# Optimization experiments

Measured on AMD Instinct MI355X. Metric: run time of the kernel, lower is better.

The kernel has to match this reference:

```python
import jax, jax.numpy as jnp
import numpy as np

B, P, V = 32, 32, 200          # batch, minPockets, vertices per pocket
NF, NT, NR, NROT = 4, 16, 5, 16
TR = NT * NR                   # 80 kernel bins
MAX_RHO = 12.0
NLIG = 7
TWO_PI = 2.0 * np.pi


def _initial_polar_grid():
    grid_rho = np.linspace(0.0, MAX_RHO, NR + 1)[1:]
    grid_theta = np.linspace(0.0, TWO_PI, NT + 1)[:-1]
    gr, gt = np.meshgrid(grid_rho, grid_theta)
    return gr.T.flatten().astype(np.float32), gt.T.flatten().astype(np.float32)


def _glorot(k, shape):
    lim = np.sqrt(6.0 / (shape[-2] + shape[-1]))
    return jax.random.uniform(k, shape, jnp.float32, -lim, lim)


def setup_inputs() -> dict:
    key = jax.random.key(0)
    ks = jax.random.split(key, 8)
    input_feat = jax.random.normal(ks[0], (B, P, V, NF), jnp.float32)
    rho_coords = jax.random.uniform(ks[1], (B, P, V, 1), jnp.float32) * MAX_RHO
    theta_coords = jax.random.uniform(ks[2], (B, P, V, 1), jnp.float32) * TWO_PI
    mask = jnp.ones((B, P, V, 1), jnp.float32)
    gr, gt = _initial_polar_grid()
    mu_rho = jnp.tile(jnp.asarray(gr)[None], (NF, 1))        # [F,TR]
    mu_theta = jnp.tile(jnp.asarray(gt)[None], (NF, 1))      # [F,TR]
    sigma_rho = jnp.full((NF, TR), MAX_RHO / 8.0, jnp.float32)
    sigma_theta = jnp.ones((NF, TR), jnp.float32)
    W_conv = _glorot(ks[3], (NF, TR, TR))
    b_conv = jnp.zeros((NF, TR), jnp.float32)
    W1 = _glorot(ks[4], (NF * TR, TR)); b1 = jnp.zeros((TR,), jnp.float32)
    W2 = _glorot(ks[5], (TR * TR, 64)); b2 = jnp.zeros((64,), jnp.float32)
    W3 = _glorot(ks[6], (64, NLIG));    b3 = jnp.zeros((NLIG,), jnp.float32)
    bn = lambda d: (jnp.ones((d,), jnp.float32), jnp.zeros((d,), jnp.float32),
                    jnp.zeros((d,), jnp.float32), jnp.ones((d,), jnp.float32))
    bn1_g, bn1_b, bn1_m, bn1_v = bn(NF * TR)
    bn2_g, bn2_b, bn2_m, bn2_v = bn(TR)
    bn3_g, bn3_b, bn3_m, bn3_v = bn(64)
    return dict(input_feat=input_feat, rho_coords=rho_coords, theta_coords=theta_coords,
                mask=mask, mu_rho=mu_rho, sigma_rho=sigma_rho, mu_theta=mu_theta,
                sigma_theta=sigma_theta, W_conv=W_conv, b_conv=b_conv, W1=W1, b1=b1,
                bn1_g=bn1_g, bn1_b=bn1_b, bn1_m=bn1_m, bn1_v=bn1_v,
                bn2_g=bn2_g, bn2_b=bn2_b, bn2_m=bn2_m, bn2_v=bn2_v,
                W2=W2, b2=b2, bn3_g=bn3_g, bn3_b=bn3_b, bn3_m=bn3_m, bn3_v=bn3_v,
                W3=W3, b3=b3)


def _bn(x, g, b, m, v, eps=1e-3):
    return (x - m) * (g * jax.lax.rsqrt(v + eps)) + b


def _conv_layer(input_feat, rho, theta, mask, mu_rho, sigma_rho, mu_theta, sigma_theta,
                W_conv, b_conv, eps=1e-5):
    # rho/theta/mask: [B,P,V,1]; mu/sigma: [F,TR]; feat: [B,P,V,F]
    # rho Gaussian is rotation-invariant -> compute once.  [B,P,V,F,TR]
    rho_g = jnp.exp(-jnp.square(rho[..., None] - mu_rho) / (jnp.square(sigma_rho) + eps))
    offs = (TWO_PI / NROT) * jnp.arange(NROT, dtype=jnp.float32)

    def step(best, off):
        th = jnp.mod(theta + off, TWO_PI)
        th_g = jnp.exp(-jnp.square(th[..., None] - mu_theta) / (jnp.square(sigma_theta) + eps))
        g = rho_g * th_g * mask[..., None]                      # [B,P,V,F,TR]
        g = g / (jnp.sum(g, axis=2, keepdims=True) + eps)       # normalize over vertices
        desc = jnp.einsum('bpvft,bpvf->bpft', g, input_feat)    # [B,P,F,TR]
        conv = jnp.einsum('bpft,ftu->bpfu', desc, W_conv) + b_conv
        return jnp.maximum(best, conv), None

    init = jnp.full((B, P, NF, TR), -jnp.inf, jnp.float32)
    best, _ = jax.lax.scan(step, init, offs)
    return best                                                  # [B,P,F,TR]


def reference(input_feat, rho_coords, theta_coords, mask, mu_rho, sigma_rho, mu_theta,
              sigma_theta, W_conv, b_conv, W1, b1, bn1_g, bn1_b, bn1_m, bn1_v,
              bn2_g, bn2_b, bn2_m, bn2_v, W2, b2, bn3_g, bn3_b, bn3_m, bn3_v, W3, b3):
    conv = _conv_layer(input_feat, rho_coords, theta_coords, mask, mu_rho, sigma_rho,
                       mu_theta, sigma_theta, W_conv, b_conv)
    x = conv.reshape(B, P, NF * TR)
    x = jax.nn.relu(_bn(x, bn1_g, bn1_b, bn1_m, bn1_v))
    x = x @ W1 + b1                                              # [B,P,TR]
    x = jax.nn.relu(_bn(x, bn2_g, bn2_b, bn2_m, bn2_v))
    cov = jnp.einsum('bpi,bpj->bij', x, x) / jnp.float32(P)      # CovarLayer [B,TR,TR]
    x = cov.reshape(B, TR * TR)
    x = jax.nn.relu(x @ W2 + b2)                                 # Dense(64, relu)
    x = _bn(x, bn3_g, bn3_b, bn3_m, bn3_v)
    return x @ W3 + b3                                           # [B, NLIG]
```

## Files before the change

kernel.cpp:

```cpp
#include <hip/hip_runtime.h>
#include <math.h>

#define B_    32
#define P_    32
#define V_    200
#define NF_   4
#define TR_   80
#define NROT_ 16
#define NLIG_ 7
#define NTH_  1024
#define PKT_  512

#define WSLOTS 33
#define CSTR   828
#define CTOT   (16 * CSTR)
#define RSTR   84
#define AUXN   5376

static constexpr float TWO_PI_F  = 6.2831854820251465f;
static constexpr float DELTA_F   = 0.39269909262657166f;

__global__ __launch_bounds__(NTH_, 4) void masif_conv_kernel(
    const float* __restrict__ feat, const float* __restrict__ rho,
    const float* __restrict__ theta, const float* __restrict__ mask,
    const float* __restrict__ mu_rho, const float* __restrict__ sigma_rho,
    const float* __restrict__ mu_theta, const float* __restrict__ sigma_theta,
    const float* __restrict__ W_conv, const float* __restrict__ b_conv,
    const float* __restrict__ W1, const float* __restrict__ b1,
    const float* __restrict__ bn1_g, const float* __restrict__ bn1_b,
    const float* __restrict__ bn1_m, const float* __restrict__ bn1_v,
    const float* __restrict__ bn2_g, const float* __restrict__ bn2_b,
    const float* __restrict__ bn2_m, const float* __restrict__ bn2_v,
    float* __restrict__ x2out)
{
    __shared__ __align__(16) float s_C[2][CTOT];
    __shared__ __align__(16) float s_aux[2][AUXN];
    __shared__ float s_mu[5], s_isr[5];
    __shared__ float s_ist1;
    __shared__ int   s_cnt[2][16], s_start[2][17];
    __shared__ int   s_whist[2][4][16];

    const int tid = threadIdx.x;
    const int pk  = tid >> 9;
    const int lt  = tid & 511;
    const int bp  = blockIdx.x * 2 + pk;
    const size_t vb = (size_t)bp * V_;

    float* Cp = s_C[pk];
    float* Ax = s_aux[pk];

    float*  stg_th  = Ax;
    float*  stg_rho = Ax + 200;
    float*  stg_msk = Ax + 400;
    float4* stg_f4  = (float4*)(Ax + 608);
    float*  Vp      = Ax + 1408;

    for (int i = lt; i < V_; i += PKT_) {
        stg_th[i]  = theta[vb + i];
        stg_rho[i] = rho[vb + i];
        stg_msk[i] = mask[vb + i];
        stg_f4[i]  = ((const float4*)(feat + vb * NF_))[i];
    }
    if (tid < 5) {
        s_mu[tid] = mu_rho[tid * 16];
        float sg = sigma_rho[tid * 16];
        s_isr[tid] = 1.0f / (sg * sg + 1e-5f);
    }
    if (tid == 5) { float sg = sigma_theta[0]; s_ist1 = 1.0f / (sg * sg + 1e-5f); }
    if (tid >= 64 && tid < 96) ((int*)s_cnt)[tid - 64] = 0;
    __syncthreads();

    int myb = 0;
    if (lt < V_) {
        float th = stg_th[lt];
        int r0 = (int)ceilf((TWO_PI_F - th) / DELTA_F);
        int lo = r0 - 2; if (lo < 1) lo = 1;
        int rs = 16;
        #pragma unroll
        for (int d = 0; d < 5; ++d) {
            int r = lo + d;
            if (r < 16 && th + (float)r * DELTA_F >= TWO_PI_F) { rs = r; break; }
        }
        myb = rs - 1;
        atomicAdd(&s_cnt[pk][myb], 1);
    }

    int rkw = 0;
    if (lt < 256) {
        const unsigned long long below = (1ULL << (tid & 63)) - 1ULL;
        const int wv = lt >> 6;
        for (int b = 0; b < 16; ++b) {
            bool p = (lt < V_) && (myb == b);
            unsigned long long m = __ballot(p);
            if (p) rkw = __popcll(m & below);
            if ((tid & 63) == b) s_whist[pk][wv][b] = __popcll(m);
        }
    }
    __syncthreads();
    if (lt == 0) {
        int run = 0;
        for (int k = 0; k < 16; ++k) { s_start[pk][k] = run; run += s_cnt[pk][k]; }
        s_start[pk][16] = run;
    }
    __syncthreads();

    {
        float4 z4 = make_float4(0.f, 0.f, 0.f, 0.f);
        float4* C4 = (float4*)Cp;
        for (int e = lt; e < CTOT / 4; e += PKT_) C4[e] = z4;
    }
    if (lt < V_) {
        int rk = rkw;
        for (int w = 0; w < (lt >> 6); ++w) rk += s_whist[pk][w][myb];
        int pos = s_start[pk][myb] + rk;
        float th = stg_th[lt];
        float mk = stg_msk[lt];
        float4 f4 = stg_f4[lt];
        float rv = stg_rho[lt];
        float R[5];
        #pragma unroll
        for (int i = 0; i < 5; ++i) {
            float d = rv - s_mu[i];
            R[i] = __expf(-d * d * s_isr[i]);
        }
        *(float4*)&Vp[pos * 12 + 0] = make_float4(R[0], R[1], R[2], R[3]);
        *(float4*)&Vp[pos * 12 + 4] = make_float4(R[4], th, f4.x * mk, f4.y * mk);
        *(float4*)&Vp[pos * 12 + 8] = make_float4(f4.z * mk, f4.w * mk, mk, 0.0f);
    }
    __syncthreads();

    {
        const int team = lt >> 5, t32 = lt & 31;
        const int w = team - 1 + t32;
        if (t32 < 20 && w >= 0 && w < WSLOTS) {
            const float ist = s_ist1;
            const float nf = (float)(team - 25 + t32);
            const int v0 = s_start[pk][team], v1 = s_start[pk][team + 1];
            float acc[25];
            #pragma unroll
            for (int i = 0; i < 25; ++i) acc[i] = 0.0f;
            for (int v = v0; v < v1; ++v) {
                float4 ra = *(const float4*)&Vp[v * 12 + 0];
                float4 rb = *(const float4*)&Vp[v * 12 + 4];
                float4 rc = *(const float4*)&Vp[v * 12 + 8];
                float q  = fmaf(nf, DELTA_F, rb.y);
                float wg = __expf(-q * q * ist);
                float R[5]  = {ra.x, ra.y, ra.z, ra.w, rb.x};
                float ch[5] = {rb.z, rb.w, rc.x, rc.y, rc.z};
                #pragma unroll
                for (int c = 0; c < 5; ++c) {
                    float t = wg * ch[c];
                    #pragma unroll
                    for (int i = 0; i < 5; ++i)
                        acc[c * 5 + i] = fmaf(t, R[i], acc[c * 5 + i]);
                }
            }
            float* dst = Cp + team * CSTR + w * 25;
            #pragma unroll
            for (int i = 0; i < 25; ++i) dst[i] = acc[i];
        }
    }
    __syncthreads();

    {
        float2* C2 = (float2*)Cp;
        for (int e = lt; e < CSTR / 2; e += PKT_) {
            float2 g[16];
            #pragma unroll
            for (int tk = 0; tk < 16; ++tk) g[tk] = C2[tk * (CSTR / 2) + e];
            #pragma unroll
            for (int tk = 1; tk < 16; ++tk) {
                g[tk].x += g[tk - 1].x; g[tk].y += g[tk - 1].y;
            }
            #pragma unroll
            for (int tk = 1; tk < 16; ++tk) C2[tk * (CSTR / 2) + e] = g[tk];
        }
    }
    __syncthreads();

    {
        const float* Tb = Cp + 15 * CSTR;
        int r   = (lt >= 320) ? 1 : 0;
        int bin = lt - r * 320;
        #pragma unroll
        for (int it = 0; it < 10; ++it) {
            const int j1  = bin & 15;
            const int ci1 = bin >> 4;
            const int c1  = (ci1 * 13) >> 6;
            const int i1  = ci1 - c1 * 5;
            const int sD = ci1, sS = 20 + i1;
            const int wT = r - j1 + 24;
            const bool pT = (wT <= 32);
            const int wTc = pT ? wT : 32;
            const float* Tp = Tb + wTc * 25;
            float tD = Tp[sD], tS = Tp[sS];
            float D = pT ? tD : 0.0f;
            float S = pT ? tS : 0.0f;
            if (r > 0) {
                const float* Cr = Cp + (r - 1) * CSTR;
                const float* Up = Cr + wTc * 25;
                float uD = Up[sD], uS = Up[sS];
                if (pT) { D -= uD; S -= uS; }
                const int wW = wT - 16;
                const bool pW = (wW >= 0);
                const int wWc = pW ? wW : 0;
                const float* Wp = Cr + wWc * 25;
                float wD = Wp[sD], wS = Wp[sS];
                if (pW) { D += wD; S += wS; }
            }
            Ax[r * (4 * RSTR) + c1 * RSTR + i1 * 16 + j1] = D / (S + 1e-5f);
            bin += 192; r += 1;
            if (bin >= 320) { bin -= 320; r += 1; }
        }
    }
    __syncthreads();

    float* s_pool2 = Cp;
    float* s_x1    = Cp + 1280;
    float* s_part  = Cp + 1600;

    if (lt < 320) {
        const int g  = lt / 80;
        const int s  = lt - g * 80;
        const int cf = s / 20;
        const int uq = s - cf * 20;
        const int u0 = uq * 4;
        const float* Wf = W_conv + (size_t)cf * TR_ * TR_ + u0;
        const float* r0 = Ax + (4 * g) * (4 * RSTR) + cf * RSTR;
        float4 a0 = make_float4(0.f, 0.f, 0.f, 0.f);
        float4 a1 = a0, a2 = a0, a3 = a0;
        #pragma unroll 4
        for (int kq = 0; kq < 20; ++kq) {
            const int k = kq * 4;
            float4 d0 = *(const float4*)&r0[k];
            float4 d1 = *(const float4*)&r0[(4 * RSTR) + k];
            float4 d2 = *(const float4*)&r0[(8 * RSTR) + k];
            float4 d3 = *(const float4*)&r0[(12 * RSTR) + k];
            float4 w0 = *(const float4*)&Wf[(size_t)(k + 0) * TR_];
            float4 w1 = *(const float4*)&Wf[(size_t)(k + 1) * TR_];
            float4 w2 = *(const float4*)&Wf[(size_t)(k + 2) * TR_];
            float4 w3 = *(const float4*)&Wf[(size_t)(k + 3) * TR_];
            a0.x = fmaf(d0.x,w0.x, fmaf(d0.y,w1.x, fmaf(d0.z,w2.x, fmaf(d0.w,w3.x, a0.x))));
            a0.y = fmaf(d0.x,w0.y, fmaf(d0.y,w1.y, fmaf(d0.z,w2.y, fmaf(d0.w,w3.y, a0.y))));
            a0.z = fmaf(d0.x,w0.z, fmaf(d0.y,w1.z, fmaf(d0.z,w2.z, fmaf(d0.w,w3.z, a0.z))));
            a0.w = fmaf(d0.x,w0.w, fmaf(d0.y,w1.w, fmaf(d0.z,w2.w, fmaf(d0.w,w3.w, a0.w))));
            a1.x = fmaf(d1.x,w0.x, fmaf(d1.y,w1.x, fmaf(d1.z,w2.x, fmaf(d1.w,w3.x, a1.x))));
            a1.y = fmaf(d1.x,w0.y, fmaf(d1.y,w1.y, fmaf(d1.z,w2.y, fmaf(d1.w,w3.y, a1.y))));
            a1.z = fmaf(d1.x,w0.z, fmaf(d1.y,w1.z, fmaf(d1.z,w2.z, fmaf(d1.w,w3.z, a1.z))));
            a1.w = fmaf(d1.x,w0.w, fmaf(d1.y,w1.w, fmaf(d1.z,w2.w, fmaf(d1.w,w3.w, a1.w))));
            a2.x = fmaf(d2.x,w0.x, fmaf(d2.y,w1.x, fmaf(d2.z,w2.x, fmaf(d2.w,w3.x, a2.x))));
            a2.y = fmaf(d2.x,w0.y, fmaf(d2.y,w1.y, fmaf(d2.z,w2.y, fmaf(d2.w,w3.y, a2.y))));
            a2.z = fmaf(d2.x,w0.z, fmaf(d2.y,w1.z, fmaf(d2.z,w2.z, fmaf(d2.w,w3.z, a2.z))));
            a2.w = fmaf(d2.x,w0.w, fmaf(d2.y,w1.w, fmaf(d2.z,w2.w, fmaf(d2.w,w3.w, a2.w))));
            a3.x = fmaf(d3.x,w0.x, fmaf(d3.y,w1.x, fmaf(d3.z,w2.x, fmaf(d3.w,w3.x, a3.x))));
            a3.y = fmaf(d3.x,w0.y, fmaf(d3.y,w1.y, fmaf(d3.z,w2.y, fmaf(d3.w,w3.y, a3.y))));
            a3.z = fmaf(d3.x,w0.z, fmaf(d3.y,w1.z, fmaf(d3.z,w2.z, fmaf(d3.w,w3.z, a3.z))));
            a3.w = fmaf(d3.x,w0.w, fmaf(d3.y,w1.w, fmaf(d3.z,w2.w, fmaf(d3.w,w3.w, a3.w))));
        }
        float4 m;
        m.x = fmaxf(fmaxf(a0.x, a1.x), fmaxf(a2.x, a3.x));
        m.y = fmaxf(fmaxf(a0.y, a1.y), fmaxf(a2.y, a3.y));
        m.z = fmaxf(fmaxf(a0.z, a1.z), fmaxf(a2.z, a3.z));
        m.w = fmaxf(fmaxf(a0.w, a1.w), fmaxf(a2.w, a3.w));
        *(float4*)&s_pool2[g * 320 + cf * TR_ + u0] = m;
    }
    __syncthreads();

    if (lt < 320) {
        float best = fmaxf(fmaxf(s_pool2[lt], s_pool2[320 + lt]),
                           fmaxf(s_pool2[640 + lt], s_pool2[960 + lt]));
        best += b_conv[lt];
        float x1 = (best - bn1_m[lt]) * (bn1_g[lt] * rsqrtf(bn1_v[lt] + 1e-3f))
                   + bn1_b[lt];
        s_x1[lt] = fmaxf(x1, 0.0f);
    }
    __syncthreads();
    for (int q = lt; q < 640; q += PKT_) {
        const int c = q / TR_;
        const int ue = q - c * TR_;
        float p = 0.0f;
        const int i0 = c * 40;
        #pragma unroll 8
        for (int i = i0; i < i0 + 40; ++i)
            p = fmaf(s_x1[i], W1[(size_t)i * TR_ + ue], p);
        s_part[q] = p;
    }
    __syncthreads();
    if (lt < TR_) {
        float h = b1[lt];
        #pragma unroll
        for (int c = 0; c < 8; ++c) h += s_part[c * TR_ + lt];
        float x2 = (h - bn2_m[lt]) * (bn2_g[lt] * rsqrtf(bn2_v[lt] + 1e-3f))
                   + bn2_b[lt];
        x2out[(size_t)bp * TR_ + lt] = fmaxf(x2, 0.0f);
    }
}

__global__ __launch_bounds__(256) void masif_head_partial(
    const float* __restrict__ x2,
    const float* __restrict__ W2,
    float* __restrict__ hpart)
{
    __shared__ __align__(16) float s_x[P_ * TR_];
    __shared__ __align__(16) float s_cov[10 * TR_];
    __shared__ float s_red[4][64];

    const int tid = threadIdx.x;
    const int b = blockIdx.x >> 3, c = blockIdx.x & 7;

    for (int i = tid; i < P_ * TR_; i += 256)
        s_x[i] = x2[(size_t)b * P_ * TR_ + i];
    __syncthreads();

    for (int o = tid; o < 800; o += 256) {
        int il = o / TR_, j = o - il * TR_;
        int i = c * 10 + il;
        float s = 0.0f;
        #pragma unroll 4
        for (int p = 0; p < P_; ++p)
            s = fmaf(s_x[p * TR_ + i], s_x[p * TR_ + j], s);
        s_cov[o] = s * (1.0f / (float)P_);
    }
    __syncthreads();

    {
        const int o = tid & 63, sub = tid >> 6;
        float acc = 0.0f;
        const int q0 = sub * 200;
        const size_t gbase = (size_t)(c * 800) * 64 + o;
        #pragma unroll 8
        for (int q = q0; q < q0 + 200; ++q)
            acc = fmaf(s_cov[q], W2[gbase + (size_t)q * 64], acc);
        s_red[sub][o] = acc;
    }
    __syncthreads();
    if (tid < 64)
        hpart[(size_t)b * 512 + c * 64 + tid] =
            s_red[0][tid] + s_red[1][tid] + s_red[2][tid] + s_red[3][tid];
}

__global__ __launch_bounds__(64) void masif_head_final(
    const float* __restrict__ hpart,
    const float* __restrict__ b2,
    const float* __restrict__ bn3_g, const float* __restrict__ bn3_b,
    const float* __restrict__ bn3_m, const float* __restrict__ bn3_v,
    const float* __restrict__ W3, const float* __restrict__ b3,
    float* __restrict__ out)
{
    __shared__ float s_h[64];
    const int tid = threadIdx.x;
    const int b = blockIdx.x;

    float h = b2[tid];
    #pragma unroll
    for (int c = 0; c < 8; ++c) h += hpart[(size_t)b * 512 + c * 64 + tid];
    h = fmaxf(h, 0.0f);
    s_h[tid] = (h - bn3_m[tid]) * (bn3_g[tid] * rsqrtf(bn3_v[tid] + 1e-3f))
               + bn3_b[tid];
    __syncthreads();

    if (tid < NLIG_) {
        float y = b3[tid];
        #pragma unroll
        for (int k = 0; k < 64; ++k)
            y = fmaf(s_h[k], W3[k * NLIG_ + tid], y);
        out[b * NLIG_ + tid] = y;
    }
}

extern "C" void kernel_launch(void* const* d_in, const int* in_sizes, int n_in,
                              void* d_out, int out_size, void* d_ws, size_t ws_size,
                              hipStream_t stream)
{
    const float* feat      = (const float*)d_in[0];
    const float* rho       = (const float*)d_in[1];
    const float* theta     = (const float*)d_in[2];
    const float* mask      = (const float*)d_in[3];
    const float* mu_rho    = (const float*)d_in[4];
    const float* sigma_rho = (const float*)d_in[5];
    const float* mu_theta  = (const float*)d_in[6];
    const float* sigma_th  = (const float*)d_in[7];
    const float* W_conv    = (const float*)d_in[8];
    const float* b_conv    = (const float*)d_in[9];
    const float* W1        = (const float*)d_in[10];
    const float* b1        = (const float*)d_in[11];
    const float* bn1_g     = (const float*)d_in[12];
    const float* bn1_b     = (const float*)d_in[13];
    const float* bn1_m     = (const float*)d_in[14];
    const float* bn1_v     = (const float*)d_in[15];
    const float* bn2_g     = (const float*)d_in[16];
    const float* bn2_b     = (const float*)d_in[17];
    const float* bn2_m     = (const float*)d_in[18];
    const float* bn2_v     = (const float*)d_in[19];
    const float* W2        = (const float*)d_in[20];
    const float* b2        = (const float*)d_in[21];
    const float* bn3_g     = (const float*)d_in[22];
    const float* bn3_b     = (const float*)d_in[23];
    const float* bn3_m     = (const float*)d_in[24];
    const float* bn3_v     = (const float*)d_in[25];
    const float* W3        = (const float*)d_in[26];
    const float* b3        = (const float*)d_in[27];

    float* x2ws  = (float*)d_ws;
    float* hpart = (float*)d_ws + (size_t)B_ * P_ * TR_;

    masif_conv_kernel<<<dim3(B_ * P_ / 2), dim3(NTH_), 0, stream>>>(
        feat, rho, theta, mask, mu_rho, sigma_rho, mu_theta, sigma_th,
        W_conv, b_conv, W1, b1,
        bn1_g, bn1_b, bn1_m, bn1_v, bn2_g, bn2_b, bn2_m, bn2_v, x2ws);

    masif_head_partial<<<dim3(B_ * 8), dim3(256), 0, stream>>>(x2ws, W2, hpart);

    masif_head_final<<<dim3(B_), dim3(64), 0, stream>>>(
        hpart, b2, bn3_g, bn3_b, bn3_m, bn3_v, W3, b3, (float*)d_out);
}
```

Baseline: 64.08 us.

## Rebalance conv accumulation and W_conv GEMM work across all block threads

The explicit zeroing pass over the accumulation buffer is removed. Out-of-band window slots are now zero-filled by the accumulation loop itself, which is rewritten as a strided loop over team/window items instead of a fixed lane mapping. The W_conv matvec-plus-max stage now spreads 2560 smaller items (2 outputs × 2 rotations each) over all 1024 threads covering both pockets, rather than 320 threads per pocket each doing 16 accumulators. This raises thread utilisation and lowers per-thread register pressure, at the cost of more index arithmetic, a wider 8-way max reduction, and repeated W_conv loads.

After: 94.06 us. 46.8% more time.

```diff
diff --git a/kernel.cpp b/kernel.cpp
--- a/kernel.cpp
+++ b/kernel.cpp
@@ -104,11 +104,6 @@
     }
     __syncthreads();
 
-    {
-        float4 z4 = make_float4(0.f, 0.f, 0.f, 0.f);
-        float4* C4 = (float4*)Cp;
-        for (int e = lt; e < CTOT / 4; e += PKT_) C4[e] = z4;
-    }
     if (lt < V_) {
         int rk = rkw;
         for (int w = 0; w < (lt >> 6); ++w) rk += s_whist[pk][w][myb];
@@ -129,12 +124,14 @@
     }
     __syncthreads();
 
-    {
-        const int team = lt >> 5, t32 = lt & 31;
-        const int w = team - 1 + t32;
-        if (t32 < 20 && w >= 0 && w < WSLOTS) {
+    for (int item = lt; item < 16 * WSLOTS; item += PKT_) {
+        const int team = item / WSLOTS;
+        const int w    = item - team * WSLOTS;
+        const int l    = w - team + 1;
+        float* dst = Cp + team * CSTR + w * 25;
+        if (l >= 0 && l < 20) {
             const float ist = s_ist1;
-            const float nf = (float)(team - 25 + t32);
+            const float nf = (float)(w - 24);
             const int v0 = s_start[pk][team], v1 = s_start[pk][team + 1];
             float acc[25];
             #pragma unroll
@@ -155,9 +152,11 @@
                         acc[c * 5 + i] = fmaf(t, R[i], acc[c * 5 + i]);
                 }
             }
-            float* dst = Cp + team * CSTR + w * 25;
             #pragma unroll
             for (int i = 0; i < 25; ++i) dst[i] = acc[i];
+        } else {
+            #pragma unroll
+            for (int i = 0; i < 25; ++i) dst[i] = 0.0f;
         }
     }
     __syncthreads();
@@ -215,64 +214,53 @@
     }
     __syncthreads();
 
-    float* s_pool2 = Cp;
-    float* s_x1    = Cp + 1280;
-    float* s_part  = Cp + 1600;
-
-    if (lt < 320) {
-        const int g  = lt / 80;
-        const int s  = lt - g * 80;
-        const int cf = s / 20;
-        const int uq = s - cf * 20;
-        const int u0 = uq * 4;
-        const float* Wf = W_conv + (size_t)cf * TR_ * TR_ + u0;
-        const float* r0 = Ax + (4 * g) * (4 * RSTR) + cf * RSTR;
-        float4 a0 = make_float4(0.f, 0.f, 0.f, 0.f);
-        float4 a1 = a0, a2 = a0, a3 = a0;
-        #pragma unroll 4
+    float* pool  = s_C[0];
+    float* x1b   = s_C[0] + 5120;
+    float* partb = s_C[0] + 5760;
+
+    for (int item = tid; item < 2560; item += NTH_) {
+        const int up  = item % 40;
+        int t = item / 40;
+        const int f   = t & 3;  t >>= 2;
+        const int g   = t & 7;  t >>= 3;
+        const int pk2 = t;
+        const int u0  = up * 2;
+        const float* r0 = s_aux[pk2] + (2 * g) * (4 * RSTR) + f * RSTR;
+        const float* r1 = r0 + (4 * RSTR);
+        const float* Wf = W_conv + (size_t)f * TR_ * TR_ + u0;
+        float a0x = 0.f, a0y = 0.f, a1x = 0.f, a1y = 0.f;
+        #pragma unroll 5
         for (int kq = 0; kq < 20; ++kq) {
             const int k = kq * 4;
             float4 d0 = *(const float4*)&r0[k];
-            float4 d1 = *(const float4*)&r0[(4 * RSTR) + k];
-            float4 d2 = *(const float4*)&r0[(8 * RSTR) + k];
-            float4 d3 = *(const float4*)&r0[(12 * RSTR) + k];
-            float4 w0 = *(const float4*)&Wf[(size_t)(k + 0) * TR_];
-            float4 w1 = *(const float4*)&Wf[(size_t)(k + 1) * TR_];
-            float4 w2 = *(const float4*)&Wf[(size_t)(k + 2) * TR_];
-            float4 w3 = *(const float4*)&Wf[(size_t)(k + 3) * TR_];
-            a0.x = fmaf(d0.x,w0.x, fmaf(d0.y,w1.x, fmaf(d0.z,w2.x, fmaf(d0.w,w3.x, a0.x))));
-            a0.y = fmaf(d0.x,w0.y, fmaf(d0.y,w1.y, fmaf(d0.z,w2.y, fmaf(d0.w,w3.y, a0.y))));
-            a0.z = fmaf(d0.x,w0.z, fmaf(d0.y,w1.z, fmaf(d0.z,w2.z, fmaf(d0.w,w3.z, a0.z))));
-            a0.w = fmaf(d0.x,w0.w, fmaf(d0.y,w1.w, fmaf(d0.z,w2.w, fmaf(d0.w,w3.w, a0.w))));
-            a1.x = fmaf(d1.x,w0.x, fmaf(d1.y,w1.x, fmaf(d1.z,w2.x, fmaf(d1.w,w3.x, a1.x))));
-            a1.y = fmaf(d1.x,w0.y, fmaf(d1.y,w1.y, fmaf(d1.z,w2.y, fmaf(d1.w,w3.y, a1.y))));
-            a1.z = fmaf(d1.x,w0.z, fmaf(d1.y,w1.z, fmaf(d1.z,w2.z, fmaf(d1.w,w3.z, a1.z))));
-            a1.w = fmaf(d1.x,w0.w, fmaf(d1.y,w1.w, fmaf(d1.z,w2.w, fmaf(d1.w,w3.w, a1.w))));
-            a2.x = fmaf(d2.x,w0.x, fmaf(d2.y,w1.x, fmaf(d2.z,w2.x, fmaf(d2.w,w3.x, a2.x))));
-            a2.y = fmaf(d2.x,w0.y, fmaf(d2.y,w1.y, fmaf(d2.z,w2.y, fmaf(d2.w,w3.y, a2.y))));
-            a2.z = fmaf(d2.x,w0.z, fmaf(d2.y,w1.z, fmaf(d2.z,w2.z, fmaf(d2.w,w3.z, a2.z))));
-            a2.w = fmaf(d2.x,w0.w, fmaf(d2.y,w1.w, fmaf(d2.z,w2.w, fmaf(d2.w,w3.w, a2.w))));
-            a3.x = fmaf(d3.x,w0.x, fmaf(d3.y,w1.x, fmaf(d3.z,w2.x, fmaf(d3.w,w3.x, a3.x))));
-            a3.y = fmaf(d3.x,w0.y, fmaf(d3.y,w1.y, fmaf(d3.z,w2.y, fmaf(d3.w,w3.y, a3.y))));
-            a3.z = fmaf(d3.x,w0.z, fmaf(d3.y,w1.z, fmaf(d3.z,w2.z, fmaf(d3.w,w3.z, a3.z))));
-            a3.w = fmaf(d3.x,w0.w, fmaf(d3.y,w1.w, fmaf(d3.z,w2.w, fmaf(d3.w,w3.w, a3.w))));
-        }
-        float4 m;
-        m.x = fmaxf(fmaxf(a0.x, a1.x), fmaxf(a2.x, a3.x));
-        m.y = fmaxf(fmaxf(a0.y, a1.y), fmaxf(a2.y, a3.y));
-        m.z = fmaxf(fmaxf(a0.z, a1.z), fmaxf(a2.z, a3.z));
-        m.w = fmaxf(fmaxf(a0.w, a1.w), fmaxf(a2.w, a3.w));
-        *(float4*)&s_pool2[g * 320 + cf * TR_ + u0] = m;
-    }
-    __syncthreads();
-
+            float4 d1 = *(const float4*)&r1[k];
+            float2 w0 = *(const float2*)&Wf[(size_t)(k + 0) * TR_];
+            float2 w1 = *(const float2*)&Wf[(size_t)(k + 1) * TR_];
+            float2 w2 = *(const float2*)&Wf[(size_t)(k + 2) * TR_];
+            float2 w3 = *(const float2*)&Wf[(size_t)(k + 3) * TR_];
+            a0x = fmaf(d0.x,w0.x, fmaf(d0.y,w1.x, fmaf(d0.z,w2.x, fmaf(d0.w,w3.x, a0x))));
+            a0y = fmaf(d0.x,w0.y, fmaf(d0.y,w1.y, fmaf(d0.z,w2.y, fmaf(d0.w,w3.y, a0y))));
+            a1x = fmaf(d1.x,w0.x, fmaf(d1.y,w1.x, fmaf(d1.z,w2.x, fmaf(d1.w,w3.x, a1x))));
+            a1y = fmaf(d1.x,w0.y, fmaf(d1.y,w1.y, fmaf(d1.z,w2.y, fmaf(d1.w,w3.y, a1y))));
+        }
+        float2 m;
+        m.x = fmaxf(a0x, a1x);
+        m.y = fmaxf(a0y, a1y);
+        *(float2*)&pool[(pk2 * 8 + g) * 320 + f * TR_ + u0] = m;
+    }
+    __syncthreads();
+
+    float* x1p = x1b + pk * 320;
+    float* ptp = partb + pk * 640;
     if (lt < 320) {
-        float best = fmaxf(fmaxf(s_pool2[lt], s_pool2[320 + lt]),
-                           fmaxf(s_pool2[640 + lt], s_pool2[960 + lt]));
+        const float* pp = pool + pk * 8 * 320 + lt;
+        float best = pp[0];
+        #pragma unroll
+        for (int g2 = 1; g2 < 8; ++g2) best = fmaxf(best, pp[g2 * 320]);
         best += b_conv[lt];
         float x1 = (best - bn1_m[lt]) * (bn1_g[lt] * rsqrtf(bn1_v[lt] + 1e-3f))
                    + bn1_b[lt];
-        s_x1[lt] = fmaxf(x1, 0.0f);
+        x1p[lt] = fmaxf(x1, 0.0f);
     }
     __syncthreads();
     for (int q = lt; q < 640; q += PKT_) {
@@ -282,14 +270,14 @@
         const int i0 = c * 40;
         #pragma unroll 8
         for (int i = i0; i < i0 + 40; ++i)
-            p = fmaf(s_x1[i], W1[(size_t)i * TR_ + ue], p);
-        s_part[q] = p;
+            p = fmaf(x1p[i], W1[(size_t)i * TR_ + ue], p);
+        ptp[q] = p;
     }
     __syncthreads();
     if (lt < TR_) {
         float h = b1[lt];
         #pragma unroll
-        for (int c = 0; c < 8; ++c) h += s_part[c * TR_ + lt];
+        for (int c = 0; c < 8; ++c) h += ptp[c * TR_ + lt];
         float x2 = (h - bn2_m[lt]) * (bn2_g[lt] * rsqrtf(bn2_v[lt] + 1e-3f))
                    + bn2_b[lt];
         x2out[(size_t)bp * TR_ + lt] = fmaxf(x2, 0.0f);
```
